# Kernel tuning notes

Hardware: AMD Instinct MI355X
Metric: run time of the kernel (lower is better)

Reference implementation:

```python
import jax, jax.numpy as jnp
import numpy as np

DIS_NORM = 6.0 * 512 / 1000.0  # 6 * D(z=0) * Nmesh / Boxsize with D(0)=1


def setup_inputs() -> dict:
    key = jax.random.key(0)
    x = jax.random.normal(key, (2, 4, 128, 128, 128), dtype=jnp.float32)
    return {"x": x}


def _lag2eul(x):
    N, C = x.shape[0], x.shape[1]
    D, H, W = x.shape[2], x.shape[3], x.shape[4]
    P = D * H * W
    Cout = C - 3 if C > 3 else 1

    # rm_dis_mean=True: mean displacement, detached
    dis_mean = jax.lax.stop_gradient(jnp.mean(x[:, :3], axis=(2, 3, 4), keepdims=True))

    pos = (x[:, :3] - dis_mean) * DIS_NORM  # (N,3,D,H,W)
    gd = jnp.arange(D, dtype=x.dtype) + 0.5
    gh = jnp.arange(H, dtype=x.dtype) + 0.5
    gw = jnp.arange(W, dtype=x.dtype) + 0.5
    grid = jnp.stack(jnp.meshgrid(gd, gh, gw, indexing='ij'))  # (3,D,H,W)
    pos = (pos + grid[None]).reshape(N, 3, P)

    if C > 3:
        val = x[:, 3:].reshape(N, Cout, P)
    else:
        val = jnp.ones((N, Cout, P), dtype=x.dtype)

    intpos = jnp.floor(pos).astype(jnp.int32)
    # 8 trilinear neighbors: bit b of n -> offset along dim b
    neighbors = (jnp.arange(8, dtype=jnp.int32)[None, :] >> jnp.arange(3, dtype=jnp.int32)[:, None]) & 1  # (3,8)
    tgt = intpos[:, :, :, None] + neighbors[None, :, None, :]  # (N,3,P,8)

    kernel = jnp.prod(1.0 - jnp.abs(pos[:, :, :, None] - tgt.astype(x.dtype)), axis=1)  # (N,P,8)
    src = val[:, :, :, None] * kernel[:, None, :, :]  # (N,Cout,P,8)

    # periodic=False: mask out-of-bounds deposits
    bounds = jnp.array([D, H, W], dtype=jnp.int32)[None, :, None, None]
    mask = jnp.all((tgt >= 0) & (tgt < bounds), axis=1)  # (N,P,8)
    ind = (tgt[:, 0] * H + tgt[:, 1]) * W + tgt[:, 2]  # (N,P,8)
    ind = jnp.clip(ind, 0, P - 1)
    src = jnp.where(mask[:, None, :, :], src, jnp.zeros((), dtype=x.dtype))

    def scatter_one(ind_n, src_n):
        mesh = jnp.zeros((Cout, P), dtype=src_n.dtype)
        return mesh.at[:, ind_n.reshape(-1)].add(src_n.reshape(Cout, -1))

    mesh = jax.vmap(scatter_one)(ind, src)  # (N,Cout,P)
    return mesh.reshape(N, Cout, D, H, W)


def reference(x):
    return _lag2eul(x)
```

## Files before the change

### kernel.cpp

```cpp
#include <hip/hip_runtime.h>
#include <hip/hip_fp16.h>

#define NBATCH 2
#define NDIM   128
#define NP     (128 * 128 * 128)
#define DIS_NORM 3.072f

#define TS   16
#define LO   5
#define HI   6
#define WIN  (TS + LO + HI)
#define WIN2 (WIN * WIN)
#define WINF (WIN * WIN * WIN)
#define TPB  8
#define NTILE (TPB * TPB * TPB)
#define NTHR 512

#define FXSCALE 16777216.0f
#define FXINV   (1.0f / 16777216.0f)

#define QCAP 1280

#define SLABH 19704

#define SUMS_OFF 0
#define SLABS_OFF 1024
#define WS_FLOATS ((size_t)SLABS_OFF + (size_t)NBATCH * NTILE * SLABH / 2)
#define WS_NEEDED_BYTES (WS_FLOATS * sizeof(float))

__device__ __constant__ int BASE27[27] = {
    0,216,792,976,1552,3088,3568,3752,4232,
    4384,4960,6496,6976,8512,12608,13888,14368,15648,
    16048,16232,16712,16864,17344,18624,19024,19176,19576};

__global__ __launch_bounds__(256) void prep_kernel(const float* __restrict__ x,
                                                   float* __restrict__ ws,
                                                   float* __restrict__ out) {
    const int plane = blockIdx.y;
    if (plane < 6) {
        const int n = plane / 3, c = plane % 3;
        const float4* xp = (const float4*)(x + ((size_t)n * 4 + c) * NP);
        float s = 0.0f;
        for (int i = blockIdx.x * 256 + threadIdx.x; i < NP / 4; i += 128 * 256) {
            float4 v = xp[i];
            s += (v.x + v.y) + (v.z + v.w);
        }
        #pragma unroll
        for (int off = 32; off > 0; off >>= 1) s += __shfl_down(s, off, 64);
        __shared__ float wsum[4];
        if ((threadIdx.x & 63) == 0) wsum[threadIdx.x >> 6] = s;
        __syncthreads();
        if (threadIdx.x == 0)
            ws[SUMS_OFF + plane * 128 + blockIdx.x] =
                (wsum[0] + wsum[1]) + (wsum[2] + wsum[3]);
    } else {
        float4* o4 = (float4*)out;
        const float4 z = make_float4(0.f, 0.f, 0.f, 0.f);
        for (int i = blockIdx.x * 256 + threadIdx.x; i < NBATCH * NP / 4; i += 128 * 256)
            o4[i] = z;
    }
}

__device__ __forceinline__ void load_means128(const float* __restrict__ ws, int n,
                                              float& m0, float& m1, float& m2) {
    float s0 = 0.f, s1 = 0.f, s2 = 0.f;
    const float* p0 = ws + SUMS_OFF + (n * 3 + 0) * 128;
    const float* p1 = ws + SUMS_OFF + (n * 3 + 1) * 128;
    const float* p2 = ws + SUMS_OFF + (n * 3 + 2) * 128;
    #pragma unroll 4
    for (int b = 0; b < 128; ++b) { s0 += p0[b]; s1 += p1[b]; s2 += p2[b]; }
    const float inv_np = 1.0f / (float)NP;
    m0 = s0 * inv_np; m1 = s1 * inv_np; m2 = s2 * inv_np;
}

__device__ __forceinline__ void deposit_pair(unsigned long long* __restrict__ winU,
                                             int b, float va, float vb) {
    const int fa = __float2int_rn(va * FXSCALE);
    const int fb = __float2int_rn(vb * FXSCALE);
    const bool odd = (b & 1);
    const long long packed = (((long long)fb) << 32) + (long long)fa;
    const long long hiOnly = ((long long)fa) << 32;
    atomicAdd(&winU[b >> 1], (unsigned long long)(odd ? hiOnly : packed));
    if (odd) atomicAdd(&winU[(b >> 1) + 1], (unsigned long long)(long long)fb);
}

__device__ __forceinline__ void slow_deposit(unsigned long long* __restrict__ winU,
                                             float* __restrict__ sp,
                                             float pd, float ph, float pw, float v,
                                             int od, int oh, int ow) {
    const float fd = floorf(pd), fh = floorf(ph), fw = floorf(pw);
    const int id = (int)fd, ih = (int)fh, iw = (int)fw;
    const float rd = pd - fd, rh = ph - fh, rw = pw - fw;
    const int wd = id - od, wh = ih - oh, ww = iw - ow;
    const float wd2[2] = {1.0f - rd, rd};
    const float wh2[2] = {1.0f - rh, rh};
    const float ww2[2] = {1.0f - rw, rw};
    #pragma unroll
    for (int dd = 0; dd < 2; ++dd) {
        const int td = id + dd, wdc = wd + dd;
        const bool dW = (unsigned)wdc < WIN, dM = (unsigned)td < NDIM;
        if (!dM && !dW) continue;
        #pragma unroll
        for (int hh = 0; hh < 2; ++hh) {
            const int th = ih + hh, whc = wh + hh;
            const bool hW = (unsigned)whc < WIN, hM = (unsigned)th < NDIM;
            const float vdh = v * wd2[dd] * wh2[hh];
            #pragma unroll
            for (int wi = 0; wi < 2; ++wi) {
                const int tw = iw + wi, wwc = ww + wi;
                const bool wW = (unsigned)wwc < WIN, wM = (unsigned)tw < NDIM;
                const float dep = vdh * ww2[wi];
                if (dW && hW && wW) {
                    const int cb = (wdc * WIN + whc) * WIN + wwc;
                    const int fx = __float2int_rn(dep * FXSCALE);
                    const long long cv = (cb & 1)
                        ? (((long long)fx) << 32) : (long long)fx;
                    atomicAdd(&winU[cb >> 1], (unsigned long long)cv);
                } else if (dM && hM && wM) {
                    atomicAdd(sp + ((size_t)td * NDIM + th) * NDIM + tw, dep);
                }
            }
        }
    }
}

__global__ __launch_bounds__(NTHR, 4) void scatter_tile_kernel(
        const float* __restrict__ x, const float* __restrict__ ws,
        __half* __restrict__ slabs, float* __restrict__ out) {
    const int blk = blockIdx.x;
    const int n = blk >> 9;
    const int t = blk & (NTILE - 1);
    const int tx = t & 7, ty = (t >> 3) & 7, tz = t >> 6;

    __shared__ ulonglong2 win2[(WINF + 3) / 4 + 1];
    __shared__ float smean[3];
    __shared__ int qcount;
    __shared__ unsigned short queue[QCAP];
    unsigned long long* winU = (unsigned long long*)win2;
    {
        float4* z4 = (float4*)win2;
        const float4 z = make_float4(0.f, 0.f, 0.f, 0.f);
        for (int i = threadIdx.x; i < (WINF + 3) / 4 + 1; i += NTHR) z4[i] = z;
        if (threadIdx.x == 0) qcount = 0;
    }
    if (threadIdx.x < 192) {
        const int c = threadIdx.x >> 6;
        const int l = threadIdx.x & 63;
        const float* p = ws + SUMS_OFF + (n * 3 + c) * 128;
        float s = p[l] + p[l + 64];
        #pragma unroll
        for (int off = 32; off > 0; off >>= 1) s += __shfl_down(s, off, 64);
        if (l == 0) smean[c] = s * (1.0f / (float)NP);
    }
    __syncthreads();
    const float m0 = smean[0], m1 = smean[1], m2 = smean[2];

    const int i0 = threadIdx.x * 8;
    const int lw0 = i0 & 15;
    const int lh  = (i0 >> 4) & 15;
    const int ld  = i0 >> 8;
    const int gd = tz * TS + ld, gh = ty * TS + lh, gw0 = tx * TS + lw0;
    const size_t prow = ((size_t)gd * NDIM + gh) * NDIM + gw0;

    const float4* x4 = (const float4*)(x + (size_t)n * 4 * NP);
    const size_t q = prow >> 2;
    const size_t s4 = NP / 4;
    float4 a0 = x4[0 * s4 + q], a1 = x4[0 * s4 + q + 1];
    float4 b0 = x4[1 * s4 + q], b1 = x4[1 * s4 + q + 1];
    float4 c0 = x4[2 * s4 + q], c1 = x4[2 * s4 + q + 1];
    float4 e0 = x4[3 * s4 + q], e1 = x4[3 * s4 + q + 1];
    const float D0[8] = {a0.x, a0.y, a0.z, a0.w, a1.x, a1.y, a1.z, a1.w};
    const float D1[8] = {b0.x, b0.y, b0.z, b0.w, b1.x, b1.y, b1.z, b1.w};
    const float D2[8] = {c0.x, c0.y, c0.z, c0.w, c1.x, c1.y, c1.z, c1.w};
    const float VV[8] = {e0.x, e0.y, e0.z, e0.w, e1.x, e1.y, e1.z, e1.w};

    const int od = tz * TS - LO, oh = ty * TS - LO, ow = tx * TS - LO;
    float* sp = out + (size_t)n * NP;

    #pragma unroll
    for (int k = 0; k < 8; ++k) {
        const float pd = (D0[k] - m0) * DIS_NORM + (float)gd + 0.5f;
        const float ph = (D1[k] - m1) * DIS_NORM + (float)gh + 0.5f;
        const float pw = (D2[k] - m2) * DIS_NORM + (float)(gw0 + k) + 0.5f;
        const float v = VV[k];

        const float fd = floorf(pd), fh = floorf(ph), fw = floorf(pw);
        const int id = (int)fd, ih = (int)fh, iw = (int)fw;
        const float rd = pd - fd, rh = ph - fh, rw = pw - fw;

        const int wd = id - od, wh = ih - oh, ww = iw - ow;
        if ((unsigned)wd <= WIN - 2 && (unsigned)wh <= WIN - 2 &&
            (unsigned)ww <= WIN - 2) {
            const int b00 = (wd * WIN + wh) * WIN + ww;
            const float sd0 = v * (1.0f - rd), sd1 = v * rd;
            const float h0 = 1.0f - rh, h1 = rh;
            const float q0 = 1.0f - rw, q1 = rw;
            deposit_pair(winU, b00,              sd0 * h0 * q0, sd0 * h0 * q1);
            deposit_pair(winU, b00 + WIN,        sd0 * h1 * q0, sd0 * h1 * q1);
            deposit_pair(winU, b00 + WIN2,       sd1 * h0 * q0, sd1 * h0 * q1);
            deposit_pair(winU, b00 + WIN2 + WIN, sd1 * h1 * q0, sd1 * h1 * q1);
        } else {
            const int qi = atomicAdd(&qcount, 1);
            if (qi < QCAP) queue[qi] = (unsigned short)(i0 + k);
            else slow_deposit(winU, sp, pd, ph, pw, v, od, oh, ow);
        }
    }

    __syncthreads();

    {
        const int nq = min(qcount, QCAP);
        const float* xb = x + (size_t)n * 4 * NP;
        for (int qi = threadIdx.x; qi < nq; qi += NTHR) {
            const int p = queue[qi];
            const int lw = p & 15, lhq = (p >> 4) & 15, ldq = p >> 8;
            const int gdq = tz * TS + ldq, ghq = ty * TS + lhq, gwq = tx * TS + lw;
            const size_t pr = ((size_t)gdq * NDIM + ghq) * NDIM + gwq;
            const float pd = (xb[pr] - m0) * DIS_NORM + (float)gdq + 0.5f;
            const float ph = (xb[(size_t)NP + pr] - m1) * DIS_NORM + (float)ghq + 0.5f;
            const float pw = (xb[2 * (size_t)NP + pr] - m2) * DIS_NORM + (float)gwq + 0.5f;
            const float v = xb[3 * (size_t)NP + pr];
            slow_deposit(winU, sp, pd, ph, pw, v, od, oh, ow);
        }
    }
    __syncthreads();

    {
        const int NU = (WINF + 1) / 2;
        for (int i = threadIdx.x; i < NU; i += NTHR) {
            const unsigned long long u = winU[i];
            const int lo = (int)(unsigned)(u & 0xffffffffull);
            const int hi = (int)(u >> 32) + (lo < 0 ? 1 : 0);
            float2 f;
            f.x = (float)lo * FXINV;
            f.y = (float)hi * FXINV;
            ((float2*)winU)[i] = f;
        }
    }
    __syncthreads();
    const float* winF = (const float*)winU;

    const int EXTY[3] = {6, 16, 5};
    const int nbase = n << 9;
    for (int r = threadIdx.x; r < WIN2; r += NTHR) {
        const int lz = r / WIN;
        const int ly = r - lz * WIN;
        int mz, pz;
        if (lz < LO) { mz = -1; pz = lz; }
        else if (lz < LO + TS) { mz = 0; pz = lz - LO; }
        else { mz = 1; pz = lz - LO - TS; }
        int my, py;
        if (ly < LO) { my = -1; py = ly; }
        else if (ly < LO + TS) { my = 0; py = ly - LO; }
        else { my = 1; py = ly - LO - TS; }
        const int dtz = tz + mz, dty = ty + my;
        if ((unsigned)dtz >= TPB || (unsigned)dty >= TPB) continue;

        const int jz = 1 - mz, jy = 1 - my;
        const int ey = EXTY[jy];
        const int rowoff = pz * ey + py;
        const int pobase = jz * 9 + jy * 3;
        const float* src = winF + r * WIN;
        const int slabRow = nbase + (dtz * 8 + dty) * 8;

        if (tx > 0) {
            __half* d = slabs + (size_t)(slabRow + tx - 1) * SLABH
                      + BASE27[pobase + 2] + rowoff * 5;
            #pragma unroll
            for (int k = 0; k < 5; ++k) d[k] = __float2half_rn(src[k]);
        }
        {
            __half* d = slabs + (size_t)(slabRow + tx) * SLABH
                      + BASE27[pobase + 1] + rowoff * 16;
            union { uint4 u; __half2 h[4]; } p0, p1;
            #pragma unroll
            for (int k = 0; k < 4; ++k)
                p0.h[k] = __floats2half2_rn(src[5 + 2 * k], src[6 + 2 * k]);
            #pragma unroll
            for (int k = 0; k < 4; ++k)
                p1.h[k] = __floats2half2_rn(src[13 + 2 * k], src[14 + 2 * k]);
            ((uint4*)d)[0] = p0.u;
            ((uint4*)d)[1] = p1.u;
        }
        if (tx < TPB - 1) {
            __half* d = slabs + (size_t)(slabRow + tx + 1) * SLABH
                      + BASE27[pobase + 0] + rowoff * 6;
            __half2* d2 = (__half2*)d;
            d2[0] = __floats2half2_rn(src[21], src[22]);
            d2[1] = __floats2half2_rn(src[23], src[24]);
            d2[2] = __floats2half2_rn(src[25], src[26]);
        }
    }
}

__device__ __forceinline__ float4 ldh4(const __half* p) {
    const uint2 u = *(const uint2*)p;
    const __half2 h0 = *(const __half2*)&u.x;
    const __half2 h1 = *(const __half2*)&u.y;
    return make_float4(__low2float(h0), __high2float(h0),
                       __low2float(h1), __high2float(h1));
}

__global__ __launch_bounds__(NTHR) void gather_tile_kernel(const __half* __restrict__ slabs,
                                                           float* __restrict__ out) {
    const int blk = blockIdx.x;
    const int n = blk >> 9;
    const int t = blk & (NTILE - 1);
    const int tx = t & 7, ty = (t >> 3) & 7, tz = t >> 6;

    const __half* __restrict__ slab = slabs + (size_t)blk * SLABH;
    float4* __restrict__ o4 = (float4*)(out + (size_t)n * NP);

    for (int i4 = threadIdx.x; i4 < TS * TS * TS / 4; i4 += NTHR) {
        const int xq = i4 & 3, y = (i4 >> 2) & 15, z = i4 >> 6;

        int ysec = 0, yp = 0, ye = 0; bool y2 = false;
        if (y < 6)        { if (ty > 0)       { ysec = 0; yp = y;      ye = 6; y2 = true; } }
        else if (y >= 11) { if (ty < TPB - 1) { ysec = 6; yp = y - 11; ye = 5; y2 = true; } }
        int zsec = 0, zp = 0; bool z2 = false;
        if (z < 6)        { if (tz > 0)       { zsec = 0;  zp = z;      z2 = true; } }
        else if (z >= 11) { if (tz < TPB - 1) { zsec = 18; zp = z - 11; z2 = true; } }

        const int rC = z * 16 + y;
        float4 s = ldh4(slab + BASE27[13] + rC * 16 + xq * 4);
        int rY = 0, rZ = 0, rYZ = 0;
        if (y2) {
            rY = z * ye + yp;
            const float4 v = ldh4(slab + BASE27[10 + ysec] + rY * 16 + xq * 4);
            s.x += v.x; s.y += v.y; s.z += v.z; s.w += v.w;
        }
        if (z2) {
            rZ = zp * 16 + y;
            const float4 v = ldh4(slab + BASE27[zsec + 4] + rZ * 16 + xq * 4);
            s.x += v.x; s.y += v.y; s.z += v.z; s.w += v.w;
            if (y2) {
                rYZ = zp * ye + yp;
                const float4 v2 = ldh4(slab + BASE27[zsec + ysec + 1] + rYZ * 16 + xq * 4);
                s.x += v2.x; s.y += v2.y; s.z += v2.z; s.w += v2.w;
            }
        }

        float se[4] = {s.x, s.y, s.z, s.w};
        #pragma unroll
        for (int e = 0; e < 4; ++e) {
            const int xx = xq * 4 + e;
            int xsec = 0, xp = 0, xe = 0; bool x2 = false;
            if (xx < 6)        { if (tx > 0)       { xsec = 0; xp = xx;      xe = 6; x2 = true; } }
            else if (xx >= 11) { if (tx < TPB - 1) { xsec = 2; xp = xx - 11; xe = 5; x2 = true; } }
            if (x2) {
                se[e] += __half2float(slab[BASE27[12 + xsec] + rC * xe + xp]);
                if (y2) se[e] += __half2float(slab[BASE27[9 + ysec + xsec] + rY * xe + xp]);
                if (z2) {
                    se[e] += __half2float(slab[BASE27[zsec + 3 + xsec] + rZ * xe + xp]);
                    if (y2) se[e] += __half2float(slab[BASE27[zsec + ysec + xsec] + rYZ * xe + xp]);
                }
            }
        }

        const size_t grow = ((size_t)(tz * TS + z) * NDIM + ty * TS + y) * (NDIM / 4)
                          + tx * 4 + xq;
        float4 o = o4[grow];
        o.x += se[0]; o.y += se[1]; o.z += se[2]; o.w += se[3];
        o4[grow] = o;
    }
}

__global__ __launch_bounds__(256) void scatter_direct_kernel(const float* __restrict__ x,
                                                             const float* __restrict__ ws,
                                                             float* __restrict__ out) {
    const int lin = blockIdx.x * 256 + threadIdx.x;
    const int n = lin >> 21;
    const int p = lin & (NP - 1);

    float m0, m1, m2;
    load_means128(ws, n, m0, m1, m2);

    const size_t base = (size_t)n * 4 * NP;
    const float d0 = x[base + 0 * (size_t)NP + p];
    const float d1 = x[base + 1 * (size_t)NP + p];
    const float d2 = x[base + 2 * (size_t)NP + p];
    const float v  = x[base + 3 * (size_t)NP + p];

    const int w = p & 127, h = (p >> 7) & 127, d = p >> 14;
    const float pd = (d0 - m0) * DIS_NORM + (float)d + 0.5f;
    const float ph = (d1 - m1) * DIS_NORM + (float)h + 0.5f;
    const float pw = (d2 - m2) * DIS_NORM + (float)w + 0.5f;
    const float fd = floorf(pd), fh = floorf(ph), fw = floorf(pw);
    const int id = (int)fd, ih = (int)fh, iw = (int)fw;
    const float rd = pd - fd, rh = ph - fh, rw = pw - fw;
    const float wd[2] = {1.0f - rd, rd}, wh[2] = {1.0f - rh, rh}, ww[2] = {1.0f - rw, rw};
    float* o = out + (size_t)n * NP;
    #pragma unroll
    for (int dd = 0; dd < 2; ++dd) {
        const int td = id + dd;
        if ((unsigned)td >= (unsigned)NDIM) continue;
        #pragma unroll
        for (int hh = 0; hh < 2; ++hh) {
            const int th = ih + hh;
            if ((unsigned)th >= (unsigned)NDIM) continue;
            const float vdh = v * wd[dd] * wh[hh];
            const int rowbase = (td * NDIM + th) * NDIM;
            #pragma unroll
            for (int wi = 0; wi < 2; ++wi) {
                const int tw = iw + wi;
                if ((unsigned)tw >= (unsigned)NDIM) continue;
                atomicAdd(o + rowbase + tw, vdh * ww[wi]);
            }
        }
    }
}

extern "C" void kernel_launch(void* const* d_in, const int* in_sizes, int n_in,
                              void* d_out, int out_size, void* d_ws, size_t ws_size,
                              hipStream_t stream) {
    const float* x = (const float*)d_in[0];
    float* out = (float*)d_out;
    float* ws = (float*)d_ws;
    __half* slabs = (__half*)(ws + SLABS_OFF);

    dim3 pgrid(128, 7);

    if (ws_size >= WS_NEEDED_BYTES) {
        prep_kernel<<<pgrid, 256, 0, stream>>>(x, ws, out);
        scatter_tile_kernel<<<dim3(NBATCH * NTILE), NTHR, 0, stream>>>(x, ws, slabs, out);
        gather_tile_kernel<<<dim3(NBATCH * NTILE), NTHR, 0, stream>>>(slabs, out);
    } else {
        prep_kernel<<<pgrid, 256, 0, stream>>>(x, ws, out);
        scatter_direct_kernel<<<dim3(NBATCH * NP / 256), 256, 0, stream>>>(x, ws, out);
    }
}
```

Baseline: 176.1 us.

## Queue particle data in LDS, fuse fixed-point decode into export, remap blocks

The overflow queue now stores each particle's computed position and value as a float4, which removes the global re-reads of x in the slow-deposit pass. QCAP shrinks so LDS use stays bounded, so overflow falls back to immediate slow deposits sooner. The separate fixed-point-to-float conversion pass and its barrier are removed; each row is decoded into registers while it is exported, which raises register pressure from the 28-float temporary. Block indices in the scatter and gather kernels are swizzled so consecutive blocks map to tiles spread by stride 128, likely to spread work across XCDs or improve L2 locality.

```diff
diff --git a/kernel.cpp b/kernel.cpp
--- a/kernel.cpp
+++ b/kernel.cpp
@@ -19,7 +19,7 @@
 #define FXSCALE 16777216.0f
 #define FXINV   (1.0f / 16777216.0f)
 
-#define QCAP 1280
+#define QCAP 176
 
 #define SLABH 19704
 
@@ -127,7 +127,7 @@
 __global__ __launch_bounds__(NTHR, 4) void scatter_tile_kernel(
         const float* __restrict__ x, const float* __restrict__ ws,
         __half* __restrict__ slabs, float* __restrict__ out) {
-    const int blk = blockIdx.x;
+    const int blk = ((blockIdx.x & 7) << 7) | (blockIdx.x >> 3);
     const int n = blk >> 9;
     const int t = blk & (NTILE - 1);
     const int tx = t & 7, ty = (t >> 3) & 7, tz = t >> 6;
@@ -135,7 +135,7 @@
     __shared__ ulonglong2 win2[(WINF + 3) / 4 + 1];
     __shared__ float smean[3];
     __shared__ int qcount;
-    __shared__ unsigned short queue[QCAP];
+    __shared__ float4 queue[QCAP];
     unsigned long long* winU = (unsigned long long*)win2;
     {
         float4* z4 = (float4*)win2;
@@ -201,7 +201,7 @@
             deposit_pair(winU, b00 + WIN2 + WIN, sd1 * h1 * q0, sd1 * h1 * q1);
         } else {
             const int qi = atomicAdd(&qcount, 1);
-            if (qi < QCAP) queue[qi] = (unsigned short)(i0 + k);
+            if (qi < QCAP) queue[qi] = make_float4(pd, ph, pw, v);
             else slow_deposit(winU, sp, pd, ph, pw, v, od, oh, ow);
         }
     }
@@ -210,35 +210,12 @@
 
     {
         const int nq = min(qcount, QCAP);
-        const float* xb = x + (size_t)n * 4 * NP;
         for (int qi = threadIdx.x; qi < nq; qi += NTHR) {
-            const int p = queue[qi];
-            const int lw = p & 15, lhq = (p >> 4) & 15, ldq = p >> 8;
-            const int gdq = tz * TS + ldq, ghq = ty * TS + lhq, gwq = tx * TS + lw;
-            const size_t pr = ((size_t)gdq * NDIM + ghq) * NDIM + gwq;
-            const float pd = (xb[pr] - m0) * DIS_NORM + (float)gdq + 0.5f;
-            const float ph = (xb[(size_t)NP + pr] - m1) * DIS_NORM + (float)ghq + 0.5f;
-            const float pw = (xb[2 * (size_t)NP + pr] - m2) * DIS_NORM + (float)gwq + 0.5f;
-            const float v = xb[3 * (size_t)NP + pr];
-            slow_deposit(winU, sp, pd, ph, pw, v, od, oh, ow);
+            const float4 e = queue[qi];
+            slow_deposit(winU, sp, e.x, e.y, e.z, e.w, od, oh, ow);
         }
     }
     __syncthreads();
-
-    {
-        const int NU = (WINF + 1) / 2;
-        for (int i = threadIdx.x; i < NU; i += NTHR) {
-            const unsigned long long u = winU[i];
-            const int lo = (int)(unsigned)(u & 0xffffffffull);
-            const int hi = (int)(u >> 32) + (lo < 0 ? 1 : 0);
-            float2 f;
-            f.x = (float)lo * FXINV;
-            f.y = (float)hi * FXINV;
-            ((float2*)winU)[i] = f;
-        }
-    }
-    __syncthreads();
-    const float* winF = (const float*)winU;
 
     const int EXTY[3] = {6, 16, 5};
     const int nbase = n << 9;
@@ -256,11 +233,24 @@
         const int dtz = tz + mz, dty = ty + my;
         if ((unsigned)dtz >= TPB || (unsigned)dty >= TPB) continue;
 
+        const int cbase = r * WIN;
+        const int w0 = cbase >> 1;
+        const int par = cbase & 1;
+        float tmp[28];
+        #pragma unroll
+        for (int wI = 0; wI < 14; ++wI) {
+            const unsigned long long u = winU[w0 + wI];
+            const int lo = (int)(unsigned)(u & 0xffffffffull);
+            const int hi = (int)(u >> 32) + (lo < 0 ? 1 : 0);
+            tmp[2 * wI]     = (float)lo * FXINV;
+            tmp[2 * wI + 1] = (float)hi * FXINV;
+        }
+        const float* src = tmp + par;
+
         const int jz = 1 - mz, jy = 1 - my;
         const int ey = EXTY[jy];
         const int rowoff = pz * ey + py;
         const int pobase = jz * 9 + jy * 3;
-        const float* src = winF + r * WIN;
         const int slabRow = nbase + (dtz * 8 + dty) * 8;
 
         if (tx > 0) {
@@ -303,7 +293,7 @@
 
 __global__ __launch_bounds__(NTHR) void gather_tile_kernel(const __half* __restrict__ slabs,
                                                            float* __restrict__ out) {
-    const int blk = blockIdx.x;
+    const int blk = ((blockIdx.x & 7) << 7) | (blockIdx.x >> 3);
     const int n = blk >> 9;
     const int t = blk & (NTILE - 1);
     const int tx = t & 7, ty = (t >> 3) & 7, tz = t >> 6;
```

Result: faster. 166.3 us (median of 2 runs) (-5.6%).
